# Optimization experiments

Hardware: AMD Instinct MI355X
Metric: run time of the kernel (lower is better)

The kernel has to match this reference:

```python
import jax, jax.numpy as jnp
import numpy as np

N_NODES = 100000
N_EDGES = 1600000
IN_DIM = 128
HID = 64


def gcn_layer(x, W, b, src, dst, n):
    # GCNConv: x' = D^{-1/2} (A + I) D^{-1/2} X W + b
    xw = x @ W  # [n, H]
    ones = jnp.ones(src.shape[0], dtype=xw.dtype)
    # degree counts incoming edges on target nodes, +1 for self-loop
    deg = jax.ops.segment_sum(ones, dst, num_segments=n) + 1.0
    dinv = jax.lax.rsqrt(deg)  # [n]
    coef = (dinv[src] * dinv[dst])[:, None]  # [E, 1]
    agg = jax.ops.segment_sum(xw[src] * coef, dst, num_segments=n)
    # self-loop contribution: dinv[i]^2 * xw[i]
    agg = agg + xw * (dinv * dinv)[:, None]
    return agg + b


def setup_inputs() -> dict:
    key = jax.random.key(0)
    ks = jax.random.split(key, 6)
    x = jax.random.normal(ks[0], (N_NODES, IN_DIM), dtype=jnp.float32)
    edge_index = jax.random.randint(ks[1], (2, N_EDGES), 0, N_NODES)
    W1 = jax.random.normal(ks[2], (IN_DIM, HID), dtype=jnp.float32) * 0.1
    b1 = jnp.zeros((HID,), dtype=jnp.float32)
    W2 = jax.random.normal(ks[3], (HID, HID), dtype=jnp.float32) * 0.1
    b2 = jnp.zeros((HID,), dtype=jnp.float32)
    Wf = jax.random.normal(ks[4], (HID, 1), dtype=jnp.float32) * 0.1
    bf = jnp.zeros((1,), dtype=jnp.float32)
    return {"x": x, "edge_index": edge_index, "W1": W1, "b1": b1,
            "W2": W2, "b2": b2, "Wf": Wf, "bf": bf}


def reference(x, edge_index, W1, b1, W2, b2, Wf, bf):
    src, dst = edge_index[0], edge_index[1]
    n = x.shape[0]
    h = jax.nn.relu(gcn_layer(x, W1, b1, src, dst, n))
    h = jax.nn.relu(gcn_layer(h, W2, b2, src, dst, n))
    g = jnp.mean(h, axis=0)  # [HID]
    return jax.nn.sigmoid(g @ Wf + bf)  # [1]
```

## Files before the change

### kernel.cpp

```cpp
#include <hip/hip_runtime.h>
#include <math.h>

static constexpr int IN_DIM = 128;
static constexpr int HID = 64;
static constexpr int BWN = 128;
static constexpr int NBP = 1024;
static constexpr int CH = 4096;
static constexpr int EPT = CH / 256;
static constexpr int CAP = 2560;
static constexpr int SMASK = 0x1FFFF;

static constexpr float DELTA1 = 0.726f;
static constexpr float DELTA2 = 0.11f;

typedef __attribute__((ext_vector_type(8))) short bf16x8;
typedef __attribute__((ext_vector_type(4))) float f32x4;

static __device__ __forceinline__ unsigned short f32_to_bf16(float f) {
    unsigned int u = __float_as_uint(f);
    u += 0x7fffu + ((u >> 16) & 1u);
    return (unsigned short)(u >> 16);
}


__global__ __launch_bounds__(256) void setupA_kernel(const int* __restrict__ dst,
                                                     int* __restrict__ bucketCnt,
                                                     const float* __restrict__ W1,
                                                     const float* __restrict__ W2,
                                                     unsigned short* __restrict__ W1f,
                                                     unsigned short* __restrict__ W2f,
                                                     int E, int nEB) {
    __shared__ int h[NBP];
    if (blockIdx.x < nEB) {
        for (int i = threadIdx.x; i < NBP; i += 256) h[i] = 0;
        __syncthreads();
        int e0 = blockIdx.x * CH;
        #pragma unroll
        for (int i = 0; i < EPT; ++i) {
            int e = e0 + i * 256 + threadIdx.x;
            if (e < E) atomicAdd(&h[dst[e] >> 7], 1);
        }
        __syncthreads();
        for (int i = threadIdx.x; i < NBP; i += 256)
            if (h[i]) atomicAdd(&bucketCnt[i], h[i]);
    } else {
        int i = (blockIdx.x - nEB) * 256 + threadIdx.x;
        if (i < IN_DIM * 64) {
            int j = i & 7, lane = (i >> 3) & 63;
            int nt = (i >> 9) & 3, kt = i >> 11;
            int k = kt * 32 + (lane >> 4) * 8 + j;
            int c = nt * 16 + (lane & 15);
            W1f[i] = f32_to_bf16(W1[k * 64 + c]);
        } else if (i < (IN_DIM + HID) * 64) {
            int i2 = i - IN_DIM * 64;
            int j = i2 & 7, lane = (i2 >> 3) & 63;
            int nt = (i2 >> 9) & 3, kt = i2 >> 11;
            int k = kt * 32 + (lane >> 4) * 8 + j;
            int c = nt * 16 + (lane & 15);
            W2f[i2] = f32_to_bf16(W2[k * 64 + c]);
        }
    }
}

__global__ void bucket_scan_kernel(const int* __restrict__ bucketCnt,
                                   int* __restrict__ bucketBase, int* __restrict__ cursor,
                                   int* __restrict__ basePad,
                                   float* __restrict__ g) {
    __shared__ int s[NBP];
    __shared__ int sp[NBP];
    int t = threadIdx.x;
    if (t < HID) g[t] = 0.f;
    int c = bucketCnt[t];
    s[t] = c;
    sp[t] = ((c + 3) & ~3) + 3 * BWN;
    __syncthreads();
    for (int off = 1; off < NBP; off <<= 1) {
        int v = (t >= off) ? s[t - off] : 0;
        int vp = (t >= off) ? sp[t - off] : 0;
        __syncthreads();
        s[t] += v;
        sp[t] += vp;
        __syncthreads();
    }
    int ex = (t == 0) ? 0 : s[t - 1];
    bucketBase[t] = ex;
    cursor[t] = ex;
    basePad[t] = (t == 0) ? 0 : sp[t - 1];
    if (t == NBP - 1) { bucketBase[NBP] = s[t]; basePad[NBP] = sp[t]; }
}

template <int K, bool IN_BF16>
__device__ __forceinline__ void gemm_body(char* smem, const void* __restrict__ Xv,
                                          const unsigned short* __restrict__ Wf,
                                          uint2* __restrict__ out, float inv_delta,
                                          int n, int blk) {
    constexpr int KT = K / 32;
    constexpr int LDSROW = K + 8;
    constexpr int GS = 65;
    unsigned short* xs = (unsigned short*)smem;
    float* grid = (float*)smem;
    int t = threadIdx.x;
    int lane = t & 63;
    int wave = t >> 6;
    int node0 = blk * 64;

    bf16x8 bfrag[KT][4];
    #pragma unroll
    for (int kt = 0; kt < KT; ++kt)
        #pragma unroll
        for (int nt = 0; nt < 4; ++nt)
            bfrag[kt][nt] = *(const bf16x8*)(Wf + ((size_t)((kt * 4 + nt) * 64 + lane)) * 8);

    if (IN_BF16) {
        const uint4* xg = (const uint4*)Xv;
        constexpr int PER = 64 * (K / 8) / 256;
        #pragma unroll
        for (int it = 0; it < PER; ++it) {
            int f = it * 256 + t;
            int nd = f / (K / 8);
            int kg = f % (K / 8);
            uint4 v = make_uint4(0, 0, 0, 0);
            if (node0 + nd < n) v = xg[(size_t)(node0 + nd) * (K / 8) + kg];
            *(uint4*)(&xs[nd * LDSROW + kg * 8]) = v;
        }
    } else {
        const float4* xg = (const float4*)Xv;
        constexpr int PER = 64 * (K / 4) / 256;
        #pragma unroll
        for (int it = 0; it < PER; ++it) {
            int f = it * 256 + t;
            int nd = f / (K / 4);
            int kg = f % (K / 4);
            float4 v = make_float4(0.f, 0.f, 0.f, 0.f);
            if (node0 + nd < n) v = xg[(size_t)(node0 + nd) * (K / 4) + kg];
            ushort4 h;
            h.x = f32_to_bf16(v.x); h.y = f32_to_bf16(v.y);
            h.z = f32_to_bf16(v.z); h.w = f32_to_bf16(v.w);
            *(ushort4*)(&xs[nd * LDSROW + kg * 4]) = h;
        }
    }
    __syncthreads();

    int m = lane & 15;
    int q = lane >> 4;
    int nrow = wave * 16 + m;
    f32x4 acc[4] = {{0.f, 0.f, 0.f, 0.f}, {0.f, 0.f, 0.f, 0.f},
                    {0.f, 0.f, 0.f, 0.f}, {0.f, 0.f, 0.f, 0.f}};
    #pragma unroll
    for (int kt = 0; kt < KT; ++kt) {
        bf16x8 afrag = *(const bf16x8*)(&xs[nrow * LDSROW + kt * 32 + q * 8]);
        #pragma unroll
        for (int nt = 0; nt < 4; ++nt)
            acc[nt] = __builtin_amdgcn_mfma_f32_16x16x32_bf16(afrag, bfrag[kt][nt], acc[nt], 0, 0, 0);
    }
    __syncthreads();
    #pragma unroll
    for (int r = 0; r < 4; ++r)
        #pragma unroll
        for (int nt = 0; nt < 4; ++nt)
            grid[(wave * 16 + q * 4 + r) * GS + nt * 16 + m] = acc[nt][r];
    __syncthreads();
    int row = t >> 2;
    int qtr = t & 3;
    const float* gr = &grid[row * GS + qtr * 16];
    unsigned lo = 0, hi = 0;
    #pragma unroll
    for (int i = 0; i < 8; ++i) {
        float q0 = rintf(fminf(fmaxf(gr[i] * inv_delta, -7.f), 7.f));
        float q1 = rintf(fminf(fmaxf(gr[8 + i] * inv_delta, -7.f), 7.f));
        lo |= ((unsigned)((int)q0 & 15)) << (4 * i);
        hi |= ((unsigned)((int)q1 & 15)) << (4 * i);
    }
    int nd = node0 + row;
    if (nd < n) out[(size_t)nd * 4 + qtr] = make_uint2(lo, hi);
}


__global__ __launch_bounds__(256) void fusedB_kernel(const int* __restrict__ src,
                                                     const int* __restrict__ dst,
                                                     int* __restrict__ cursor,
                                                     int* __restrict__ bucketArr,
                                                     const float* __restrict__ x,
                                                     const unsigned short* __restrict__ W1f,
                                                     uint2* __restrict__ xw, float inv_delta,
                                                     int n, int E, int nEB) {
    __shared__ alignas(16) char smem[64 * (IN_DIM + 8) * 2];
    if (blockIdx.x < nEB) {
        int* h = (int*)smem;
        int* gbase = h + NBP;
        for (int i = threadIdx.x; i < NBP; i += 256) h[i] = 0;
        __syncthreads();
        int e0 = blockIdx.x * CH;
        int s_[EPT], d_[EPT], p_[EPT];
        #pragma unroll
        for (int i = 0; i < EPT; ++i) {
            int e = e0 + i * 256 + threadIdx.x;
            if (e < E) {
                s_[i] = src[e];
                d_[i] = dst[e];
                p_[i] = atomicAdd(&h[d_[i] >> 7], 1);
            } else {
                d_[i] = -1;
            }
        }
        __syncthreads();
        for (int i = threadIdx.x; i < NBP; i += 256) {
            int c = h[i];
            gbase[i] = c ? atomicAdd(&cursor[i], c) : 0;
        }
        __syncthreads();
        #pragma unroll
        for (int i = 0; i < EPT; ++i) {
            if (d_[i] >= 0) {
                int b = d_[i] >> 7;
                bucketArr[(size_t)gbase[b] + p_[i]] = s_[i] | ((d_[i] & 127) << 17);
            }
        }
    } else {
        gemm_body<IN_DIM, false>(smem, x, W1f, xw, inv_delta, n, blockIdx.x - nEB);
    }
}

__global__ __launch_bounds__(256) void gemm2_kernel(const void* __restrict__ Xv,
                                                    const unsigned short* __restrict__ Wf,
                                                    uint2* __restrict__ out, float inv_delta,
                                                    int n) {
    __shared__ alignas(16) char smem[64 * 65 * 4];
    gemm_body<HID, true>(smem, Xv, Wf, out, inv_delta, n, blockIdx.x);
}


__global__ __launch_bounds__(256) void csrpass_kernel(const int* __restrict__ bucketArr,
                                                      const int* __restrict__ bucketBase,
                                                      const int* __restrict__ basePad,
                                                      int* __restrict__ rowInfo,
                                                      float* __restrict__ dinv,
                                                      int* __restrict__ col, int n) {
    __shared__ int stage[CAP];
    __shared__ int posArr[CAP];
    __shared__ int nodeCnt[BWN];
    __shared__ int nodeIncl[BWN];
    int b = blockIdx.x;
    int node0 = b * BWN;
    int eBeg = bucketBase[b], eEnd = bucketBase[b + 1];
    int pBeg = basePad[b];
    int cnt = eEnd - eBeg;
    if (cnt > CAP) cnt = CAP;
    for (int i = threadIdx.x; i < BWN; i += 256) nodeCnt[i] = 0;
    __syncthreads();
    for (int i = threadIdx.x; i < cnt; i += 256) {
        int v = bucketArr[eBeg + i];
        stage[i] = v;
        posArr[i] = atomicAdd(&nodeCnt[v >> 17], 1);
    }
    __syncthreads();
    int padc = 0;
    if (threadIdx.x < BWN) {
        padc = (nodeCnt[threadIdx.x] + 3) & ~3;
        nodeIncl[threadIdx.x] = padc;
    }
    __syncthreads();
    for (int off = 1; off < BWN; off <<= 1) {
        int v = 0;
        if (threadIdx.x < BWN && threadIdx.x >= off) v = nodeIncl[threadIdx.x - off];
        __syncthreads();
        if (threadIdx.x < BWN) nodeIncl[threadIdx.x] += v;
        __syncthreads();
    }
    int node = node0 + threadIdx.x;
    if (threadIdx.x < BWN && node < n) {
        int incl = nodeIncl[threadIdx.x];
        int c = nodeCnt[threadIdx.x];
        int rs = pBeg + incl - padc;
        int nb = padc >> 2;
        if (nb > 255) nb = 255;
        rowInfo[node] = (rs << 8) | nb;
        dinv[node] = rsqrtf((float)c + 1.0f);
        for (int p = c; p < padc; ++p) col[rs + p] = -1;
    }
    __syncthreads();
    for (int i = threadIdx.x; i < cnt; i += 256) {
        int v = stage[i];
        int ln = v >> 17;
        int padl = (nodeCnt[ln] + 3) & ~3;
        col[pBeg + (nodeIncl[ln] - padl) + posArr[i]] = v & SMASK;
    }
}


__global__ __launch_bounds__(256) void enrich_kernel(int* __restrict__ col,
                                                     const float* __restrict__ dinv,
                                                     int total, int n) {
    int stride = gridDim.x * 256;
    for (int e = blockIdx.x * 256 + threadIdx.x; e < total; e += stride) {
        int v = col[e];
        int out = 0;
        if (v >= 0) {
            int s = v & SMASK;
            int sc = s < n ? s : 0;
            float d = dinv[sc];
            float qf = fminf(d * 32768.f, 32767.f);
            unsigned q = (unsigned)(qf + 0.5f);
            out = s | (int)(q << 17);
        }
        col[e] = out;
    }
}


static __device__ __forceinline__ void i4_fma16(uint2 w, float c, float* a) {
    #pragma unroll
    for (int k = 0; k < 8; ++k) {
        int q0 = ((int)(w.x << (28 - 4 * k))) >> 28;
        int q1 = ((int)(w.y << (28 - 4 * k))) >> 28;
        a[k]     = fmaf(c, (float)q0, a[k]);
        a[8 + k] = fmaf(c, (float)q1, a[8 + k]);
    }
}

template <bool FUSE_REDUCE>
__global__ __launch_bounds__(256) void agg_kernel(const uint2* __restrict__ xw,
                                                  const int* __restrict__ col,
                                                  const int* __restrict__ rowInfo,
                                                  const float* __restrict__ dinv,
                                                  const float* __restrict__ bias,
                                                  float delta,
                                                  unsigned short* __restrict__ outb,
                                                  float* __restrict__ gsum, int n) {
    __shared__ float wacc[4][HID];
    int lane = threadIdx.x & 63;
    int wave = threadIdx.x >> 6;
    int grp = lane >> 2;
    int li = lane & 3;
    int node = (blockIdx.x * 4 + wave) * 16 + grp;
    bool act = node < n;
    float r[16];
    #pragma unroll
    for (int k = 0; k < 16; ++k) r[k] = 0.f;
    if (act) {
        unsigned info = (unsigned)rowInfo[node];
        int nb = (int)(info & 255u);
        const int4* cp = (const int4*)(col + (info >> 8));
        float ddn = dinv[node];
        float dsc = ddn * 3.0517578125e-05f;
        float a[16];
        #pragma unroll
        for (int k = 0; k < 16; ++k) a[k] = 0.f;
        if (nb > 0) {
            uint2 wA[4];
            float fA[4];
            {
                int4 c0 = cp[0];
                unsigned u0 = c0.x, u1 = c0.y, u2 = c0.z, u3 = c0.w;
                wA[0] = xw[(size_t)(u0 & SMASK) * 4 + li]; fA[0] = (float)(u0 >> 17) * dsc;
                wA[1] = xw[(size_t)(u1 & SMASK) * 4 + li]; fA[1] = (float)(u1 >> 17) * dsc;
                wA[2] = xw[(size_t)(u2 & SMASK) * 4 + li]; fA[2] = (float)(u2 >> 17) * dsc;
                wA[3] = xw[(size_t)(u3 & SMASK) * 4 + li]; fA[3] = (float)(u3 >> 17) * dsc;
            }
            int4 cN = cp[nb > 1 ? 1 : 0];
            for (int b = 1; b < nb; ++b) {
                unsigned u0 = cN.x, u1 = cN.y, u2 = cN.z, u3 = cN.w;
                cN = cp[b + 1 < nb ? b + 1 : b];
                uint2 wB[4];
                float fB[4];
                wB[0] = xw[(size_t)(u0 & SMASK) * 4 + li]; fB[0] = (float)(u0 >> 17) * dsc;
                wB[1] = xw[(size_t)(u1 & SMASK) * 4 + li]; fB[1] = (float)(u1 >> 17) * dsc;
                wB[2] = xw[(size_t)(u2 & SMASK) * 4 + li]; fB[2] = (float)(u2 >> 17) * dsc;
                wB[3] = xw[(size_t)(u3 & SMASK) * 4 + li]; fB[3] = (float)(u3 >> 17) * dsc;
                __builtin_amdgcn_sched_barrier(0);
                #pragma unroll
                for (int k = 0; k < 4; ++k) i4_fma16(wA[k], fA[k], a);
                #pragma unroll
                for (int k = 0; k < 4; ++k) { wA[k] = wB[k]; fA[k] = fB[k]; }
            }
            #pragma unroll
            for (int k = 0; k < 4; ++k) i4_fma16(wA[k], fA[k], a);
        }
        uint2 ws = xw[(size_t)node * 4 + li];
        i4_fma16(ws, ddn * ddn, a);
        const float4* b4 = (const float4*)bias;
        #pragma unroll
        for (int p = 0; p < 4; ++p) {
            float4 bb = b4[li * 4 + p];
            r[p * 4 + 0] = fmaxf(fmaf(a[p * 4 + 0], delta, bb.x), 0.f);
            r[p * 4 + 1] = fmaxf(fmaf(a[p * 4 + 1], delta, bb.y), 0.f);
            r[p * 4 + 2] = fmaxf(fmaf(a[p * 4 + 2], delta, bb.z), 0.f);
            r[p * 4 + 3] = fmaxf(fmaf(a[p * 4 + 3], delta, bb.w), 0.f);
        }
    }
    if (!FUSE_REDUCE) {
        if (act) {
            uint4 o0, o1;
            o0.x = (unsigned)f32_to_bf16(r[0])  | ((unsigned)f32_to_bf16(r[1])  << 16);
            o0.y = (unsigned)f32_to_bf16(r[2])  | ((unsigned)f32_to_bf16(r[3])  << 16);
            o0.z = (unsigned)f32_to_bf16(r[4])  | ((unsigned)f32_to_bf16(r[5])  << 16);
            o0.w = (unsigned)f32_to_bf16(r[6])  | ((unsigned)f32_to_bf16(r[7])  << 16);
            o1.x = (unsigned)f32_to_bf16(r[8])  | ((unsigned)f32_to_bf16(r[9])  << 16);
            o1.y = (unsigned)f32_to_bf16(r[10]) | ((unsigned)f32_to_bf16(r[11]) << 16);
            o1.z = (unsigned)f32_to_bf16(r[12]) | ((unsigned)f32_to_bf16(r[13]) << 16);
            o1.w = (unsigned)f32_to_bf16(r[14]) | ((unsigned)f32_to_bf16(r[15]) << 16);
            ((uint4*)outb)[(size_t)node * 8 + li * 2]     = o0;
            ((uint4*)outb)[(size_t)node * 8 + li * 2 + 1] = o1;
        }
        return;
    }
    #pragma unroll
    for (int k = 0; k < 16; ++k) {
        float v = r[k];
        v += __shfl_xor(v, 4);
        v += __shfl_xor(v, 8);
        v += __shfl_xor(v, 16);
        v += __shfl_xor(v, 32);
        r[k] = v;
    }
    if (lane < 4) {
        #pragma unroll
        for (int k = 0; k < 16; ++k) wacc[wave][li * 16 + k] = r[k];
    }
    __syncthreads();
    if (threadIdx.x < HID) {
        float s = wacc[0][threadIdx.x] + wacc[1][threadIdx.x] +
                  wacc[2][threadIdx.x] + wacc[3][threadIdx.x];
        atomicAdd(&gsum[threadIdx.x], s);
    }
}

__global__ void final_kernel(const float* __restrict__ g, const float* __restrict__ Wf,
                             const float* __restrict__ bf, float* __restrict__ out,
                             float inv_n) {
    int lane = threadIdx.x;
    float v = g[lane] * inv_n * Wf[lane];
    #pragma unroll
    for (int off = 32; off > 0; off >>= 1) v += __shfl_down(v, off);
    if (lane == 0) out[0] = 1.f / (1.f + expf(-(v + bf[0])));
}


extern "C" void kernel_launch(void* const* d_in, const int* in_sizes, int n_in,
                              void* d_out, int out_size, void* d_ws, size_t ws_size,
                              hipStream_t stream) {
    const float* x = (const float*)d_in[0];
    const int* edge_index = (const int*)d_in[1];
    const float* W1 = (const float*)d_in[2];
    const float* b1 = (const float*)d_in[3];
    const float* W2 = (const float*)d_in[4];
    const float* b2 = (const float*)d_in[5];
    const float* Wf = (const float*)d_in[6];
    const float* bf = (const float*)d_in[7];

    const int n = in_sizes[0] / IN_DIM;
    const int E = in_sizes[1] / 2;
    const int* src = edge_index;
    const int* dst = edge_index + E;
    const int NB = (n + BWN - 1) / BWN;
    const int nEB = (E + CH - 1) / CH;
    const int gblocks = (n + 63) / 64;
    const int wblocks = ((IN_DIM + HID) * 64 + 255) / 256;
    const int colCap = E + NBP * (3 * BWN + 8);

    char* p = (char*)d_ws;
    auto carve = [&](size_t bytes) -> void* {
        void* r = (void*)p;
        p += (bytes + 255) & ~(size_t)255;
        return r;
    };
    int* bucketCnt  = (int*)carve((size_t)NBP * 4);
    int* bucketBase = (int*)carve((size_t)(NBP + 1) * 4);
    int* cursor     = (int*)carve((size_t)NBP * 4);
    int* basePad    = (int*)carve((size_t)(NBP + 1) * 4);
    int* rowInfo    = (int*)carve((size_t)n * 4);
    float* dinv     = (float*)carve((size_t)n * 4);
    int* bucketArr  = (int*)carve((size_t)E * 4);
    int* col        = (int*)carve((size_t)colCap * 4);
    unsigned short* W1f = (unsigned short*)carve((size_t)IN_DIM * 64 * 2);
    unsigned short* W2f = (unsigned short*)carve((size_t)HID * 64 * 2);
    uint2* xw       = (uint2*)carve((size_t)n * 32);
    unsigned short* h1  = (unsigned short*)carve((size_t)n * HID * 2);
    float* g        = (float*)carve(HID * 4);

    hipMemsetAsync(bucketCnt, 0, (size_t)NBP * 4, stream);
    setupA_kernel<<<nEB + wblocks, 256, 0, stream>>>(dst, bucketCnt, W1, W2, W1f, W2f, E, nEB);
    bucket_scan_kernel<<<1, NBP, 0, stream>>>(bucketCnt, bucketBase, cursor, basePad, g);
    fusedB_kernel<<<nEB + gblocks, 256, 0, stream>>>(src, dst, cursor, bucketArr,
                                                     x, W1f, xw, 1.0f / DELTA1, n, E, nEB);
    csrpass_kernel<<<NB, 256, 0, stream>>>(bucketArr, bucketBase, basePad, rowInfo, dinv, col, n);
    enrich_kernel<<<2048, 256, 0, stream>>>(col, dinv, colCap, n);
    agg_kernel<false><<<(n + 63) / 64, 256, 0, stream>>>(xw, col, rowInfo, dinv, b1,
                                                         DELTA1, h1, nullptr, n);
    gemm2_kernel<<<gblocks, 256, 0, stream>>>(h1, W2f, xw, 1.0f / DELTA2, n);
    agg_kernel<true><<<(n + 63) / 64, 256, 0, stream>>>(xw, col, rowInfo, dinv, b2,
                                                        DELTA2, nullptr, g, n);
    final_kernel<<<1, 64, 0, stream>>>(g, Wf, bf, (float*)d_out, 1.0f / (float)n);
}
```

Before: 244.0 us.

## Fuse layer-1 aggregation with layer-2 GEMM and use persistent aggregation kernels

Merges the first aggregation kernel with the second-layer GEMM. Each tile's aggregated bf16 rows are staged in LDS and multiplied by W2 with MFMA, so the intermediate h1 buffer is no longer written to or read back from global memory. Both aggregation kernels become persistent grid-stride loops with a fixed block count, and they prefetch the next tile's row info. The second aggregation accumulates per-thread partial sums across tiles, which cuts the number of atomic reductions. The cost is extra barriers per tile and fewer blocks in flight, which may hurt latency hiding for the gather.

```diff
diff --git a/kernel.cpp b/kernel.cpp
--- a/kernel.cpp
+++ b/kernel.cpp
@@ -9,6 +9,7 @@
 static constexpr int EPT = CH / 256;
 static constexpr int CAP = 2560;
 static constexpr int SMASK = 0x1FFFF;
+static constexpr int AGB = 521;
 
 static constexpr float DELTA1 = 0.726f;
 static constexpr float DELTA2 = 0.11f;
@@ -89,7 +90,7 @@
     if (t == NBP - 1) { bucketBase[NBP] = s[t]; basePad[NBP] = sp[t]; }
 }
 
-template <int K, bool IN_BF16>
+template <int K>
 __device__ __forceinline__ void gemm_body(char* smem, const void* __restrict__ Xv,
                                           const unsigned short* __restrict__ Wf,
                                           uint2* __restrict__ out, float inv_delta,
@@ -111,19 +112,7 @@
         for (int nt = 0; nt < 4; ++nt)
             bfrag[kt][nt] = *(const bf16x8*)(Wf + ((size_t)((kt * 4 + nt) * 64 + lane)) * 8);
 
-    if (IN_BF16) {
-        const uint4* xg = (const uint4*)Xv;
-        constexpr int PER = 64 * (K / 8) / 256;
-        #pragma unroll
-        for (int it = 0; it < PER; ++it) {
-            int f = it * 256 + t;
-            int nd = f / (K / 8);
-            int kg = f % (K / 8);
-            uint4 v = make_uint4(0, 0, 0, 0);
-            if (node0 + nd < n) v = xg[(size_t)(node0 + nd) * (K / 8) + kg];
-            *(uint4*)(&xs[nd * LDSROW + kg * 8]) = v;
-        }
-    } else {
+    {
         const float4* xg = (const float4*)Xv;
         constexpr int PER = 64 * (K / 4) / 256;
         #pragma unroll
@@ -217,16 +206,8 @@
             }
         }
     } else {
-        gemm_body<IN_DIM, false>(smem, x, W1f, xw, inv_delta, n, blockIdx.x - nEB);
-    }
-}
-
-__global__ __launch_bounds__(256) void gemm2_kernel(const void* __restrict__ Xv,
-                                                    const unsigned short* __restrict__ Wf,
-                                                    uint2* __restrict__ out, float inv_delta,
-                                                    int n) {
-    __shared__ alignas(16) char smem[64 * 65 * 4];
-    gemm_body<HID, true>(smem, Xv, Wf, out, inv_delta, n, blockIdx.x);
+        gemm_body<IN_DIM>(smem, x, W1f, xw, inv_delta, n, blockIdx.x - nEB);
+    }
 }
 
 
@@ -318,78 +299,113 @@
     }
 }
 
-template <bool FUSE_REDUCE>
-__global__ __launch_bounds__(256) void agg_kernel(const uint2* __restrict__ xw,
-                                                  const int* __restrict__ col,
-                                                  const int* __restrict__ rowInfo,
-                                                  const float* __restrict__ dinv,
-                                                  const float* __restrict__ bias,
-                                                  float delta,
-                                                  unsigned short* __restrict__ outb,
-                                                  float* __restrict__ gsum, int n) {
-    __shared__ float wacc[4][HID];
-    int lane = threadIdx.x & 63;
-    int wave = threadIdx.x >> 6;
-    int grp = lane >> 2;
-    int li = lane & 3;
-    int node = (blockIdx.x * 4 + wave) * 16 + grp;
-    bool act = node < n;
-    float r[16];
-    #pragma unroll
-    for (int k = 0; k < 16; ++k) r[k] = 0.f;
-    if (act) {
-        unsigned info = (unsigned)rowInfo[node];
-        int nb = (int)(info & 255u);
-        const int4* cp = (const int4*)(col + (info >> 8));
-        float ddn = dinv[node];
-        float dsc = ddn * 3.0517578125e-05f;
-        float a[16];
-        #pragma unroll
-        for (int k = 0; k < 16; ++k) a[k] = 0.f;
-        if (nb > 0) {
-            uint2 wA[4];
-            float fA[4];
-            {
-                int4 c0 = cp[0];
-                unsigned u0 = c0.x, u1 = c0.y, u2 = c0.z, u3 = c0.w;
-                wA[0] = xw[(size_t)(u0 & SMASK) * 4 + li]; fA[0] = (float)(u0 >> 17) * dsc;
-                wA[1] = xw[(size_t)(u1 & SMASK) * 4 + li]; fA[1] = (float)(u1 >> 17) * dsc;
-                wA[2] = xw[(size_t)(u2 & SMASK) * 4 + li]; fA[2] = (float)(u2 >> 17) * dsc;
-                wA[3] = xw[(size_t)(u3 & SMASK) * 4 + li]; fA[3] = (float)(u3 >> 17) * dsc;
-            }
-            int4 cN = cp[nb > 1 ? 1 : 0];
-            for (int b = 1; b < nb; ++b) {
-                unsigned u0 = cN.x, u1 = cN.y, u2 = cN.z, u3 = cN.w;
-                cN = cp[b + 1 < nb ? b + 1 : b];
-                uint2 wB[4];
-                float fB[4];
-                wB[0] = xw[(size_t)(u0 & SMASK) * 4 + li]; fB[0] = (float)(u0 >> 17) * dsc;
-                wB[1] = xw[(size_t)(u1 & SMASK) * 4 + li]; fB[1] = (float)(u1 >> 17) * dsc;
-                wB[2] = xw[(size_t)(u2 & SMASK) * 4 + li]; fB[2] = (float)(u2 >> 17) * dsc;
-                wB[3] = xw[(size_t)(u3 & SMASK) * 4 + li]; fB[3] = (float)(u3 >> 17) * dsc;
-                __builtin_amdgcn_sched_barrier(0);
-                #pragma unroll
-                for (int k = 0; k < 4; ++k) i4_fma16(wA[k], fA[k], a);
-                #pragma unroll
-                for (int k = 0; k < 4; ++k) { wA[k] = wB[k]; fA[k] = fB[k]; }
-            }
+static __device__ __forceinline__ void agg_row(const uint2* __restrict__ xw,
+                                               const int* __restrict__ col,
+                                               unsigned info, float ddn,
+                                               int li, int node, float* a) {
+    int nb = (int)(info & 255u);
+    const int4* cp = (const int4*)(col + (info >> 8));
+    float dsc = ddn * 3.0517578125e-05f;
+    #pragma unroll
+    for (int k = 0; k < 16; ++k) a[k] = 0.f;
+    if (nb > 0) {
+        uint2 wA[4];
+        float fA[4];
+        {
+            int4 c0 = cp[0];
+            unsigned u0 = c0.x, u1 = c0.y, u2 = c0.z, u3 = c0.w;
+            wA[0] = xw[(size_t)(u0 & SMASK) * 4 + li]; fA[0] = (float)(u0 >> 17) * dsc;
+            wA[1] = xw[(size_t)(u1 & SMASK) * 4 + li]; fA[1] = (float)(u1 >> 17) * dsc;
+            wA[2] = xw[(size_t)(u2 & SMASK) * 4 + li]; fA[2] = (float)(u2 >> 17) * dsc;
+            wA[3] = xw[(size_t)(u3 & SMASK) * 4 + li]; fA[3] = (float)(u3 >> 17) * dsc;
+        }
+        int4 cN = cp[nb > 1 ? 1 : 0];
+        for (int b = 1; b < nb; ++b) {
+            unsigned u0 = cN.x, u1 = cN.y, u2 = cN.z, u3 = cN.w;
+            cN = cp[b + 1 < nb ? b + 1 : b];
+            uint2 wB[4];
+            float fB[4];
+            wB[0] = xw[(size_t)(u0 & SMASK) * 4 + li]; fB[0] = (float)(u0 >> 17) * dsc;
+            wB[1] = xw[(size_t)(u1 & SMASK) * 4 + li]; fB[1] = (float)(u1 >> 17) * dsc;
+            wB[2] = xw[(size_t)(u2 & SMASK) * 4 + li]; fB[2] = (float)(u2 >> 17) * dsc;
+            wB[3] = xw[(size_t)(u3 & SMASK) * 4 + li]; fB[3] = (float)(u3 >> 17) * dsc;
+            __builtin_amdgcn_sched_barrier(0);
             #pragma unroll
             for (int k = 0; k < 4; ++k) i4_fma16(wA[k], fA[k], a);
-        }
-        uint2 ws = xw[(size_t)node * 4 + li];
-        i4_fma16(ws, ddn * ddn, a);
-        const float4* b4 = (const float4*)bias;
-        #pragma unroll
-        for (int p = 0; p < 4; ++p) {
-            float4 bb = b4[li * 4 + p];
-            r[p * 4 + 0] = fmaxf(fmaf(a[p * 4 + 0], delta, bb.x), 0.f);
-            r[p * 4 + 1] = fmaxf(fmaf(a[p * 4 + 1], delta, bb.y), 0.f);
-            r[p * 4 + 2] = fmaxf(fmaf(a[p * 4 + 2], delta, bb.z), 0.f);
-            r[p * 4 + 3] = fmaxf(fmaf(a[p * 4 + 3], delta, bb.w), 0.f);
-        }
-    }
-    if (!FUSE_REDUCE) {
+            #pragma unroll
+            for (int k = 0; k < 4; ++k) { wA[k] = wB[k]; fA[k] = fB[k]; }
+        }
+        #pragma unroll
+        for (int k = 0; k < 4; ++k) i4_fma16(wA[k], fA[k], a);
+    }
+    uint2 ws = xw[(size_t)node * 4 + li];
+    i4_fma16(ws, ddn * ddn, a);
+}
+
+
+__global__ __launch_bounds__(256) void aggGemm_kernel(const uint2* __restrict__ xwin,
+                                                      const int* __restrict__ col,
+                                                      const int* __restrict__ rowInfo,
+                                                      const float* __restrict__ dinv,
+                                                      const float* __restrict__ bias,
+                                                      const unsigned short* __restrict__ W2f,
+                                                      uint2* __restrict__ xwout,
+                                                      float delta, float inv_delta2, int n) {
+    __shared__ alignas(16) char smem[64 * 65 * 4];
+    constexpr int LR2 = HID + 8;
+    unsigned short* xs = (unsigned short*)smem;
+    float* grid = (float*)smem;
+    int t = threadIdx.x;
+    int lane = t & 63, wave = t >> 6;
+    int grp = lane >> 2, li = lane & 3;
+    int m = lane & 15, q = lane >> 4;
+    int ro = wave * 16 + grp;
+
+    bf16x8 bfrag[2][4];
+    #pragma unroll
+    for (int kt = 0; kt < 2; ++kt)
+        #pragma unroll
+        for (int nt = 0; nt < 4; ++nt)
+            bfrag[kt][nt] = *(const bf16x8*)(W2f + ((size_t)((kt * 4 + nt) * 64 + lane)) * 8);
+
+    const float4* b4 = (const float4*)bias;
+    float4 bb[4];
+    #pragma unroll
+    for (int p = 0; p < 4; ++p) bb[p] = b4[li * 4 + p];
+
+    int ntiles = (n + 63) >> 6;
+    int tile = blockIdx.x;
+    unsigned infoC = 0;
+    float dC = 0.f;
+    if (tile < ntiles) {
+        int nodeC = tile * 64 + ro;
+        if (nodeC < n) { infoC = (unsigned)rowInfo[nodeC]; dC = dinv[nodeC]; }
+    }
+    for (; tile < ntiles; tile += gridDim.x) {
+        int node = tile * 64 + ro;
+        bool act = node < n;
+        int tileN = tile + gridDim.x;
+        unsigned infoN = 0;
+        float dN = 0.f;
+        if (tileN < ntiles) {
+            int nodeN = tileN * 64 + ro;
+            if (nodeN < n) { infoN = (unsigned)rowInfo[nodeN]; dN = dinv[nodeN]; }
+        }
+        float r[16];
+        #pragma unroll
+        for (int k = 0; k < 16; ++k) r[k] = 0.f;
         if (act) {
+            float a[16];
+            agg_row(xwin, col, infoC, dC, li, node, a);
+            #pragma unroll
+            for (int p = 0; p < 4; ++p) {
+                r[p * 4 + 0] = fmaxf(fmaf(a[p * 4 + 0], delta, bb[p].x), 0.f);
+                r[p * 4 + 1] = fmaxf(fmaf(a[p * 4 + 1], delta, bb[p].y), 0.f);
+                r[p * 4 + 2] = fmaxf(fmaf(a[p * 4 + 2], delta, bb[p].z), 0.f);
+                r[p * 4 + 3] = fmaxf(fmaf(a[p * 4 + 3], delta, bb[p].w), 0.f);
+            }
+        }
+        {
             uint4 o0, o1;
             o0.x = (unsigned)f32_to_bf16(r[0])  | ((unsigned)f32_to_bf16(r[1])  << 16);
             o0.y = (unsigned)f32_to_bf16(r[2])  | ((unsigned)f32_to_bf16(r[3])  << 16);
@@ -399,29 +415,119 @@
             o1.y = (unsigned)f32_to_bf16(r[10]) | ((unsigned)f32_to_bf16(r[11]) << 16);
             o1.z = (unsigned)f32_to_bf16(r[12]) | ((unsigned)f32_to_bf16(r[13]) << 16);
             o1.w = (unsigned)f32_to_bf16(r[14]) | ((unsigned)f32_to_bf16(r[15]) << 16);
-            ((uint4*)outb)[(size_t)node * 8 + li * 2]     = o0;
-            ((uint4*)outb)[(size_t)node * 8 + li * 2 + 1] = o1;
-        }
-        return;
+            *(uint4*)(&xs[ro * LR2 + li * 16])     = o0;
+            *(uint4*)(&xs[ro * LR2 + li * 16 + 8]) = o1;
+        }
+        __syncthreads();
+        int nrow = wave * 16 + m;
+        f32x4 acc[4] = {{0.f, 0.f, 0.f, 0.f}, {0.f, 0.f, 0.f, 0.f},
+                        {0.f, 0.f, 0.f, 0.f}, {0.f, 0.f, 0.f, 0.f}};
+        #pragma unroll
+        for (int kt = 0; kt < 2; ++kt) {
+            bf16x8 afrag = *(const bf16x8*)(&xs[nrow * LR2 + kt * 32 + q * 8]);
+            #pragma unroll
+            for (int nt = 0; nt < 4; ++nt)
+                acc[nt] = __builtin_amdgcn_mfma_f32_16x16x32_bf16(afrag, bfrag[kt][nt], acc[nt], 0, 0, 0);
+        }
+        __syncthreads();
+        #pragma unroll
+        for (int rr = 0; rr < 4; ++rr)
+            #pragma unroll
+            for (int nt = 0; nt < 4; ++nt)
+                grid[(wave * 16 + q * 4 + rr) * 65 + nt * 16 + m] = acc[nt][rr];
+        __syncthreads();
+        int row = t >> 2;
+        int qtr = t & 3;
+        const float* gr = &grid[row * 65 + qtr * 16];
+        unsigned lo = 0, hi = 0;
+        #pragma unroll
+        for (int i = 0; i < 8; ++i) {
+            float q0 = rintf(fminf(fmaxf(gr[i] * inv_delta2, -7.f), 7.f));
+            float q1 = rintf(fminf(fmaxf(gr[8 + i] * inv_delta2, -7.f), 7.f));
+            lo |= ((unsigned)((int)q0 & 15)) << (4 * i);
+            hi |= ((unsigned)((int)q1 & 15)) << (4 * i);
+        }
+        int nd = tile * 64 + row;
+        if (nd < n) xwout[(size_t)nd * 4 + qtr] = make_uint2(lo, hi);
+        __syncthreads();
+        infoC = infoN;
+        dC = dN;
+    }
+}
+
+
+__global__ __launch_bounds__(256) void agg2_kernel(const uint2* __restrict__ xw,
+                                                   const int* __restrict__ col,
+                                                   const int* __restrict__ rowInfo,
+                                                   const float* __restrict__ dinv,
+                                                   const float* __restrict__ bias,
+                                                   float delta,
+                                                   float* __restrict__ gsum, int n) {
+    __shared__ float wacc[4][HID];
+    int t = threadIdx.x;
+    int lane = t & 63, wave = t >> 6;
+    int grp = lane >> 2, li = lane & 3;
+    int wgid = blockIdx.x * 4 + wave;
+    int nw = gridDim.x * 4;
+    int ntasks = (n + 15) >> 4;
+
+    const float4* b4 = (const float4*)bias;
+    float4 bb[4];
+    #pragma unroll
+    for (int p = 0; p < 4; ++p) bb[p] = b4[li * 4 + p];
+
+    float racc[16];
+    #pragma unroll
+    for (int k = 0; k < 16; ++k) racc[k] = 0.f;
+
+    int task = wgid;
+    unsigned infoC = 0;
+    float dC = 0.f;
+    if (task < ntasks) {
+        int nodeC = task * 16 + grp;
+        if (nodeC < n) { infoC = (unsigned)rowInfo[nodeC]; dC = dinv[nodeC]; }
+    }
+    for (; task < ntasks; task += nw) {
+        int node = task * 16 + grp;
+        bool act = node < n;
+        int taskN = task + nw;
+        unsigned infoN = 0;
+        float dN = 0.f;
+        if (taskN < ntasks) {
+            int nodeN = taskN * 16 + grp;
+            if (nodeN < n) { infoN = (unsigned)rowInfo[nodeN]; dN = dinv[nodeN]; }
+        }
+        if (act) {
+            float a[16];
+            agg_row(xw, col, infoC, dC, li, node, a);
+            #pragma unroll
+            for (int p = 0; p < 4; ++p) {
+                racc[p * 4 + 0] += fmaxf(fmaf(a[p * 4 + 0], delta, bb[p].x), 0.f);
+                racc[p * 4 + 1] += fmaxf(fmaf(a[p * 4 + 1], delta, bb[p].y), 0.f);
+                racc[p * 4 + 2] += fmaxf(fmaf(a[p * 4 + 2], delta, bb[p].z), 0.f);
+                racc[p * 4 + 3] += fmaxf(fmaf(a[p * 4 + 3], delta, bb[p].w), 0.f);
+            }
+        }
+        infoC = infoN;
+        dC = dN;
     }
     #pragma unroll
     for (int k = 0; k < 16; ++k) {
-        float v = r[k];
+        float v = racc[k];
         v += __shfl_xor(v, 4);
         v += __shfl_xor(v, 8);
         v += __shfl_xor(v, 16);
         v += __shfl_xor(v, 32);
-        r[k] = v;
+        racc[k] = v;
     }
     if (lane < 4) {
         #pragma unroll
-        for (int k = 0; k < 16; ++k) wacc[wave][li * 16 + k] = r[k];
-    }
-    __syncthreads();
-    if (threadIdx.x < HID) {
-        float s = wacc[0][threadIdx.x] + wacc[1][threadIdx.x] +
-                  wacc[2][threadIdx.x] + wacc[3][threadIdx.x];
-        atomicAdd(&gsum[threadIdx.x], s);
+        for (int k = 0; k < 16; ++k) wacc[wave][li * 16 + k] = racc[k];
+    }
+    __syncthreads();
+    if (t < HID) {
+        float s = wacc[0][t] + wacc[1][t] + wacc[2][t] + wacc[3][t];
+        atomicAdd(&gsum[t], s);
     }
 }
 
@@ -457,6 +563,8 @@
     const int gblocks = (n + 63) / 64;
     const int wblocks = ((IN_DIM + HID) * 64 + 255) / 256;
     const int colCap = E + NBP * (3 * BWN + 8);
+    const int ntiles = (n + 63) / 64;
+    const int ab1 = ntiles < AGB ? ntiles : AGB;
 
     char* p = (char*)d_ws;
     auto carve = [&](size_t bytes) -> void* {
@@ -475,7 +583,7 @@
     unsigned short* W1f = (unsigned short*)carve((size_t)IN_DIM * 64 * 2);
     unsigned short* W2f = (unsigned short*)carve((size_t)HID * 64 * 2);
     uint2* xw       = (uint2*)carve((size_t)n * 32);
-    unsigned short* h1  = (unsigned short*)carve((size_t)n * HID * 2);
+    uint2* xw2      = (uint2*)carve((size_t)n * 32);
     float* g        = (float*)carve(HID * 4);
 
     hipMemsetAsync(bucketCnt, 0, (size_t)NBP * 4, stream);
@@ -485,10 +593,8 @@
                                                      x, W1f, xw, 1.0f / DELTA1, n, E, nEB);
     csrpass_kernel<<<NB, 256, 0, stream>>>(bucketArr, bucketBase, basePad, rowInfo, dinv, col, n);
     enrich_kernel<<<2048, 256, 0, stream>>>(col, dinv, colCap, n);
-    agg_kernel<false><<<(n + 63) / 64, 256, 0, stream>>>(xw, col, rowInfo, dinv, b1,
-                                                         DELTA1, h1, nullptr, n);
-    gemm2_kernel<<<gblocks, 256, 0, stream>>>(h1, W2f, xw, 1.0f / DELTA2, n);
-    agg_kernel<true><<<(n + 63) / 64, 256, 0, stream>>>(xw, col, rowInfo, dinv, b2,
-                                                        DELTA2, nullptr, g, n);
+    aggGemm_kernel<<<ab1, 256, 0, stream>>>(xw, col, rowInfo, dinv, b1, W2f, xw2,
+                                            DELTA1, 1.0f / DELTA2, n);
+    agg2_kernel<<<AGB, 256, 0, stream>>>(xw2, col, rowInfo, dinv, b2, DELTA2, g, n);
     final_kernel<<<1, 64, 0, stream>>>(g, Wf, bf, (float*)d_out, 1.0f / (float)n);
 }
```

After: 232.7 us. -4.7%, faster.
